# Kernel tuning notes

Hardware: AMD Instinct MI355X
Metric: run time of the kernel (lower is better)

Reference implementation:

```python
import jax, jax.numpy as jnp
import numpy as np

MODES = 256
WIDTH = 64
T_HIST = 1
T_FUT = 1
BATCH = 64
S = 8192


def setup_inputs() -> dict:
    key = jax.random.key(0)
    ks = jax.random.split(key, 12)
    scale = 1.0 / (WIDTH * WIDTH)
    inp = {
        "u": jax.random.normal(ks[0], (BATCH, S, T_HIST), dtype=jnp.float32),
        # lifting layer: Linear(T_HIST+1 -> WIDTH), stored [in, out]
        "fc0_w": jax.random.normal(ks[1], (T_HIST + 1, WIDTH), dtype=jnp.float32) * 0.5,
        "fc0_b": jax.random.normal(ks[2], (WIDTH,), dtype=jnp.float32) * 0.1,
        # 4 spectral conv layers, complex weights stored as real/imag parts
        "sw_r": scale * jax.random.uniform(ks[3], (4, WIDTH, WIDTH, MODES), dtype=jnp.float32),
        "sw_i": scale * jax.random.uniform(ks[4], (4, WIDTH, WIDTH, MODES), dtype=jnp.float32),
        # 4 pointwise (1x1 conv) layers: weight [out,in], bias [out]
        "pw_w": jax.random.normal(ks[5], (4, WIDTH, WIDTH), dtype=jnp.float32) * (1.0 / np.sqrt(WIDTH)),
        "pw_b": jax.random.normal(ks[6], (4, WIDTH), dtype=jnp.float32) * 0.1,
        # projection head
        "fc1_w": jax.random.normal(ks[7], (WIDTH, 128), dtype=jnp.float32) * (1.0 / np.sqrt(WIDTH)),
        "fc1_b": jax.random.normal(ks[8], (128,), dtype=jnp.float32) * 0.1,
        "fc2_w": jax.random.normal(ks[9], (128, T_FUT), dtype=jnp.float32) * (1.0 / np.sqrt(128)),
        "fc2_b": jax.random.normal(ks[10], (T_FUT,), dtype=jnp.float32) * 0.1,
    }
    return inp


def _spectral_conv(x, wr, wi):
    # x: [b, c_in, s] real; weights: [c_in, c_out, MODES] (real/imag parts)
    s = x.shape[-1]
    xf = jnp.fft.rfft(x)                     # [b, c_in, s//2+1] complex
    w = wr + 1j * wi
    om = jnp.einsum('bix,iox->box', xf[:, :, :MODES], w)  # [b, c_out, MODES]
    out_ft = jnp.zeros((x.shape[0], wr.shape[1], s // 2 + 1), dtype=om.dtype)
    out_ft = out_ft.at[:, :, :MODES].set(om)
    return jnp.fft.irfft(out_ft, n=s)        # [b, c_out, s] real


def reference(u, fc0_w, fc0_b, sw_r, sw_i, pw_w, pw_b, fc1_w, fc1_b, fc2_w, fc2_b):
    b, s, _ = u.shape
    grid = jnp.broadcast_to(jnp.linspace(0.0, 1.0, s, dtype=u.dtype)[None, :, None], (b, s, 1))
    x = jnp.concatenate([u, grid], axis=-1)              # [b, s, 2]
    x = x @ fc0_w + fc0_b                                # [b, s, W]
    x = jnp.transpose(x, (0, 2, 1))                      # [b, W, s]
    for l in range(4):
        x1 = _spectral_conv(x, sw_r[l], sw_i[l])
        x2 = jnp.einsum('oi,bis->bos', pw_w[l], x) + pw_b[l][None, :, None]
        x = x1 + x2
        if l < 3:
            x = jax.nn.gelu(x, approximate=False)
    x = jnp.transpose(x, (0, 2, 1))                      # [b, s, W]
    x = jax.nn.gelu(x @ fc1_w + fc1_b, approximate=False)
    x = x @ fc2_w + fc2_b                                # [b, s, T_FUT]
    return x
```

## Files before the change

kernel.cpp:

```cpp
#include <hip/hip_runtime.h>
#include <hip/hip_bf16.h>
#include <math.h>

#define BB 64
#define CC 64
#define SS 8192
#define HS 4096
#define NMODE 256
#define KK2 512

typedef __attribute__((ext_vector_type(8))) short short8;
typedef __attribute__((ext_vector_type(16))) float f32x16;

__device__ __forceinline__ float gelu_exact(float v) {
    return 0.5f * v * (1.0f + erff(v * 0.7071067811865476f));
}
__device__ __forceinline__ float b2f(ushort u) {
    return __uint_as_float(((unsigned int)u) << 16);
}
__device__ __forceinline__ ushort f2b(float v) {
    __hip_bfloat16 h = __float2bfloat16(v);
    return *(ushort*)&h;
}
__device__ __forceinline__ void split2(float v, ushort& h, ushort& l) {
    h = f2b(v);
    l = f2b(v - b2f(h));
}
__device__ __forceinline__ int colk(int c) {
    return (c < 256) ? (c & ~1) : (((c - 256) & ~1) | 1);
}
__device__ __forceinline__ void dma16(const ushort* g, ushort* l) {
    __builtin_amdgcn_global_load_lds((const __attribute__((address_space(1))) void*)g,
                                     (__attribute__((address_space(3))) void*)l, 16, 0, 0);
}

__global__ void build_T1p(ushort* __restrict__ h, ushort* __restrict__ l) {
    int c = blockIdx.x;
    int n = blockIdx.y * 256 + threadIdx.x;
    int k = colk(c), ri = c & 1;
    int m = (n * k) & (SS - 1);
    float th = (float)m * (6.283185307179586476925f / (float)SS);
    float s, co;
    sincosf(th, &s, &co);
    float v = ri ? -s : co;
    ushort hh, ll;
    split2(v, hh, ll);
    h[(size_t)c * HS + n] = hh;
    l[(size_t)c * HS + n] = ll;
}

__global__ void build_T2r(ushort* __restrict__ h, ushort* __restrict__ l) {
    int n = blockIdx.x;
    int c = blockIdx.y * 256 + threadIdx.x;
    int k = colk(c), ri = c & 1;
    int m = (n * k) & (SS - 1);
    float th = (float)m * (6.283185307179586476925f / (float)SS);
    float s, co;
    sincosf(th, &s, &co);
    float v = ri ? -s : co;
    ushort hh, ll;
    split2(v, hh, ll);
    h[(size_t)n * KK2 + c] = hh;
    l[(size_t)n * KK2 + c] = ll;
}

__global__ void zero_xf(float* __restrict__ p) {
    size_t i = ((size_t)blockIdx.x * 256 + threadIdx.x) * 4;
    *(float4*)&p[i] = make_float4(0.f, 0.f, 0.f, 0.f);
}

__global__ void lift_kernel(const float* __restrict__ u, const float* __restrict__ w0,
                            const float* __restrict__ b0, ushort* __restrict__ Eh,
                            ushort* __restrict__ El, ushort* __restrict__ Oh,
                            ushort* __restrict__ Ol) {
    int n = blockIdx.x * 256 + threadIdx.x;
    int c = blockIdx.y;
    int b = blockIdx.z;
    float g1 = (float)n * (1.0f / (float)(SS - 1));
    float g2 = (float)(n + HS) * (1.0f / (float)(SS - 1));
    float v1 = u[b * SS + n] * w0[c] + g1 * w0[CC + c] + b0[c];
    float v2 = u[b * SS + n + HS] * w0[c] + g2 * w0[CC + c] + b0[c];
    float E = v1 + v2, O = v1 - v2;
    ushort hh, ll;
    size_t idx = (size_t)(b * CC + c) * HS + n;
    split2(E, hh, ll);
    Eh[idx] = hh;
    El[idx] = ll;
    split2(O, hh, ll);
    Oh[idx] = hh;
    Ol[idx] = ll;
}

__global__ __launch_bounds__(256, 3) void dft_mfma(
    const ushort* __restrict__ Eh, const ushort* __restrict__ El,
    const ushort* __restrict__ Oh, const ushort* __restrict__ Ol,
    const ushort* __restrict__ t1h, const ushort* __restrict__ t1l,
    float* __restrict__ Xf) {
    __shared__ __align__(16) ushort SM[16384];
    ushort* As_h = SM;
    ushort* As_l = SM + 4096;
    ushort* Bs_h = SM + 8192;
    ushort* Bs_l = SM + 12288;
    const int t = threadIdx.x;
    const int L = blockIdx.x;
    const int gq = L >> 5, j = L & 31;
    const int c0 = (j >> 3) * 128;
    const int m0 = ((gq & 3) * 8 + (j & 7)) * 128;
    const int kz = (gq >> 2) * 1024;
    const ushort* __restrict__ Ahp = (c0 < 256) ? Eh : Oh;
    const ushort* __restrict__ Alp = (c0 < 256) ? El : Ol;
    const int lane = t & 63, w = t >> 6;
    const int wm = (w >> 1) * 64, wn = (w & 1) * 64;
    const int l32 = lane & 31, lh = lane >> 5;
    const int sr = t >> 1, sh = (t & 1) * 16;
    const int g0 = (t & 1) * 2;
    const int d0 = ((g0 + 0) * 128 + sr) * 8;
    const int d1 = ((g0 + 1) * 128 + sr) * 8;

    f32x16 acc[2][2];
#pragma unroll
    for (int i = 0; i < 2; i++)
#pragma unroll
        for (int jj = 0; jj < 2; jj++) acc[i][jj] = (f32x16)0.f;

    const size_t arow = (size_t)(m0 + sr) * HS;
    const size_t brow = (size_t)(c0 + sr) * HS;
    const int kend = kz + 1024;

    short8 a0h, a1h, a0l, a1l, b0h, b1h, b0l, b1l;
    {
        const size_t ga = arow + kz + sh;
        const size_t gb = brow + kz + sh;
        a0h = *(const short8*)&Ahp[ga];
        a1h = *(const short8*)&Ahp[ga + 8];
        a0l = *(const short8*)&Alp[ga];
        a1l = *(const short8*)&Alp[ga + 8];
        b0h = *(const short8*)&t1h[gb];
        b1h = *(const short8*)&t1h[gb + 8];
        b0l = *(const short8*)&t1l[gb];
        b1l = *(const short8*)&t1l[gb + 8];
    }
    for (int kt = kz; kt < kend; kt += 32) {
        __syncthreads();
        *(short8*)&As_h[d0] = a0h;
        *(short8*)&As_h[d1] = a1h;
        *(short8*)&As_l[d0] = a0l;
        *(short8*)&As_l[d1] = a1l;
        *(short8*)&Bs_h[d0] = b0h;
        *(short8*)&Bs_h[d1] = b1h;
        *(short8*)&Bs_l[d0] = b0l;
        *(short8*)&Bs_l[d1] = b1l;
        __syncthreads();
        const int ktn = (kt + 32 < kend) ? kt + 32 : kz;
        const size_t ga = arow + ktn + sh;
        const size_t gb = brow + ktn + sh;
        a0h = *(const short8*)&Ahp[ga];
        a1h = *(const short8*)&Ahp[ga + 8];
        a0l = *(const short8*)&Alp[ga];
        a1l = *(const short8*)&Alp[ga + 8];
        b0h = *(const short8*)&t1h[gb];
        b1h = *(const short8*)&t1h[gb + 8];
        b0l = *(const short8*)&t1l[gb];
        b1l = *(const short8*)&t1l[gb + 8];
#pragma unroll
        for (int s2 = 0; s2 < 2; s2++) {
            const int kg = s2 * 2 + lh;
            short8 ah[2], al[2], bh2[2], bl2[2];
#pragma unroll
            for (int mt = 0; mt < 2; mt++) {
                int off = (kg * 128 + wm + mt * 32 + l32) * 8;
                ah[mt] = *(const short8*)&As_h[off];
                al[mt] = *(const short8*)&As_l[off];
            }
#pragma unroll
            for (int nt = 0; nt < 2; nt++) {
                int off = (kg * 128 + wn + nt * 32 + l32) * 8;
                bh2[nt] = *(const short8*)&Bs_h[off];
                bl2[nt] = *(const short8*)&Bs_l[off];
            }
#pragma unroll
            for (int nt = 0; nt < 2; nt++)
#pragma unroll
                for (int mt = 0; mt < 2; mt++) {
                    acc[mt][nt] = __builtin_amdgcn_mfma_f32_32x32x16_bf16(ah[mt], bh2[nt], acc[mt][nt], 0, 0, 0);
                    acc[mt][nt] = __builtin_amdgcn_mfma_f32_32x32x16_bf16(ah[mt], bl2[nt], acc[mt][nt], 0, 0, 0);
                    acc[mt][nt] = __builtin_amdgcn_mfma_f32_32x32x16_bf16(al[mt], bh2[nt], acc[mt][nt], 0, 0, 0);
                }
        }
    }
#pragma unroll
    for (int mt = 0; mt < 2; mt++)
#pragma unroll
        for (int nt = 0; nt < 2; nt++) {
            int col = c0 + wn + nt * 32 + l32;
#pragma unroll
            for (int reg = 0; reg < 16; reg++) {
                int row = m0 + wm + mt * 32 + (reg & 3) + 8 * (reg >> 2) + 4 * lh;
                atomicAdd(&Xf[(size_t)row * KK2 + col], acc[mt][nt][reg]);
            }
        }
}

__global__ __launch_bounds__(256) void mode_mix(const float* __restrict__ Xf,
                                                const float* __restrict__ swr,
                                                const float* __restrict__ swi,
                                                ushort* __restrict__ omh,
                                                ushort* __restrict__ oml, int l) {
    int k = threadIdx.x;
    int bg = blockIdx.x * 2;
    int og = blockIdx.y * 2;
    const int cp = ((k & 1) << 8) | ((k >> 1) << 1);
    float ar[2][2] = {}, ai[2][2] = {};
#pragma unroll 2
    for (int i = 0; i < CC; i++) {
        float2 x0 = *(const float2*)&Xf[((size_t)(bg + 0) * CC + i) * KK2 + cp];
        float2 x1 = *(const float2*)&Xf[((size_t)(bg + 1) * CC + i) * KK2 + cp];
        size_t wb = ((size_t)(l * CC + i) * CC + og) * NMODE + k;
        float wr0 = swr[wb], wi0 = swi[wb];
        float wr1 = swr[wb + NMODE], wi1 = swi[wb + NMODE];
        ar[0][0] += x0.x * wr0 - x0.y * wi0;
        ai[0][0] += x0.x * wi0 + x0.y * wr0;
        ar[0][1] += x0.x * wr1 - x0.y * wi1;
        ai[0][1] += x0.x * wi1 + x0.y * wr1;
        ar[1][0] += x1.x * wr0 - x1.y * wi0;
        ai[1][0] += x1.x * wi0 + x1.y * wr0;
        ar[1][1] += x1.x * wr1 - x1.y * wi1;
        ai[1][1] += x1.x * wi1 + x1.y * wr1;
    }
    float ck = (k == 0) ? (1.0f / (float)SS) : (2.0f / (float)SS);
#pragma unroll
    for (int b2 = 0; b2 < 2; b2++)
#pragma unroll
        for (int oo = 0; oo < 2; oo++) {
            float re = ar[b2][oo] * ck;
            float im = ai[b2][oo] * ck;
            ushort hr, lr2, hi2, li2;
            split2(re, hr, lr2);
            split2(im, hi2, li2);
            size_t base = ((size_t)(bg + b2) * CC + og + oo) * KK2 + cp;
            *(ushort2*)&omh[base] = make_ushort2(hr, hi2);
            *(ushort2*)&oml[base] = make_ushort2(lr2, li2);
        }
}

__global__ __launch_bounds__(256, 2) void inv_mfma(
    const ushort* __restrict__ omh, const ushort* __restrict__ oml,
    const ushort* __restrict__ t2h, const ushort* __restrict__ t2l,
    const float* __restrict__ pww, const float* __restrict__ pwb,
    ushort* __restrict__ Eh, ushort* __restrict__ El,
    ushort* __restrict__ Oh, ushort* __restrict__ Ol, int l, int gel) {
    __shared__ __align__(16) ushort SM[16384];
    ushort* As_h = SM;
    ushort* As_l = SM + 4096;
    ushort* Bs_h = SM + 8192;
    ushort* Bs_l = SM + 12288;
    const int t = threadIdx.x;
    const int n0 = blockIdx.x * 128;
    const int row0 = blockIdx.y * 128;
    const int lane = t & 63, w = t >> 6;
    const int wm = (w >> 1) * 64, wn = (w & 1) * 64;
    const int l32 = lane & 31, lh = lane >> 5;

    f32x16 aP[2][2], aQ[2][2];
#pragma unroll
    for (int i = 0; i < 2; i++)
#pragma unroll
        for (int jj = 0; jj < 2; jj++) {
            aP[i][jj] = (f32x16)0.f;
            aQ[i][jj] = (f32x16)0.f;
        }

    const size_t aoff = (size_t)(row0 + lane) * KK2 + w * 8;
    const size_t boff = (size_t)(n0 + lane) * KK2 + w * 8;
    const size_t rstep = (size_t)64 * KK2;
    ushort* dAh = As_h + w * 1024;
    ushort* dAl = As_l + w * 1024;
    ushort* dBh = Bs_h + w * 1024;
    ushort* dBl = Bs_l + w * 1024;

#pragma unroll
    for (int half = 0; half < 2; half++) {
        for (int hs8 = 0; hs8 < 8; hs8++) {
            const int kt = half * 256 + hs8 * 32;
            dma16(omh + aoff + kt, dAh);
            dma16(omh + aoff + rstep + kt, dAh + 512);
            dma16(oml + aoff + kt, dAl);
            dma16(oml + aoff + rstep + kt, dAl + 512);
            dma16(t2h + boff + kt, dBh);
            dma16(t2h + boff + rstep + kt, dBh + 512);
            dma16(t2l + boff + kt, dBl);
            dma16(t2l + boff + rstep + kt, dBl + 512);
            __syncthreads();
#pragma unroll
            for (int s2 = 0; s2 < 2; s2++) {
                const int kg = s2 * 2 + lh;
                short8 ah[2], al[2], bh2[2], bl2[2];
#pragma unroll
                for (int mt = 0; mt < 2; mt++) {
                    int off = (kg * 128 + wm + mt * 32 + l32) * 8;
                    ah[mt] = *(const short8*)&As_h[off];
                    al[mt] = *(const short8*)&As_l[off];
                }
#pragma unroll
                for (int nt = 0; nt < 2; nt++) {
                    int off = (kg * 128 + wn + nt * 32 + l32) * 8;
                    bh2[nt] = *(const short8*)&Bs_h[off];
                    bl2[nt] = *(const short8*)&Bs_l[off];
                }
#pragma unroll
                for (int nt = 0; nt < 2; nt++)
#pragma unroll
                    for (int mt = 0; mt < 2; mt++) {
                        f32x16* ac = half ? &aQ[mt][nt] : &aP[mt][nt];
                        *ac = __builtin_amdgcn_mfma_f32_32x32x16_bf16(ah[mt], bh2[nt], *ac, 0, 0, 0);
                        *ac = __builtin_amdgcn_mfma_f32_32x32x16_bf16(ah[mt], bl2[nt], *ac, 0, 0, 0);
                        *ac = __builtin_amdgcn_mfma_f32_32x32x16_bf16(al[mt], bh2[nt], *ac, 0, 0, 0);
                    }
            }
            __syncthreads();
        }
    }
#pragma unroll
    for (int mt = 0; mt < 2; mt++)
#pragma unroll
        for (int nt = 0; nt < 2; nt++) {
            f32x16 p = aP[mt][nt];
            aP[mt][nt] = p + aQ[mt][nt];
            aQ[mt][nt] = p - aQ[mt][nt];
        }
    short8 pah[4][2], pal[4][2];
#pragma unroll
    for (int ks = 0; ks < 4; ks++)
#pragma unroll
        for (int mt = 0; mt < 2; mt++) {
            const float* pp = &pww[(size_t)(l * CC + mt * 32 + l32) * CC + ks * 16 + lh * 8];
            float4 pa = *(const float4*)pp;
            float4 pb = *(const float4*)(pp + 4);
            float pv[8] = {pa.x, pa.y, pa.z, pa.w, pb.x, pb.y, pb.z, pb.w};
#pragma unroll
            for (int e = 0; e < 8; e++) {
                ushort h2, l2;
                split2(0.5f * pv[e], h2, l2);
                pah[ks][mt][e] = (short)h2;
                pal[ks][mt][e] = (short)l2;
            }
        }
    const size_t xsrc = (size_t)(row0 + (w >> 1) * 64 + (w & 1) * 32 + (lane >> 4)) * HS +
                        n0 + (lane & 15) * 8;
    ushort* dX = SM + w * 4096;
    const int bsw = w >> 1;
    const ushort* const srcs[4] = {Eh, El, Oh, Ol};
#pragma unroll
    for (int r = 0; r < 4; r++) {
        const ushort* src = srcs[r];
        const bool isO = (r >= 2), isHi = !(r & 1);
        __syncthreads();
#pragma unroll
        for (int q = 0; q < 8; q++) dma16(src + xsrc + (size_t)q * 4 * HS, dX + q * 512);
        __syncthreads();
#pragma unroll
        for (int ks = 0; ks < 4; ks++) {
            short8 bf[2], nbf[2];
#pragma unroll
            for (int nt = 0; nt < 2; nt++) {
                const int rb = (bsw * 64 + ks * 16 + lh * 8) * 128 + wn + nt * 32 + l32;
#pragma unroll
                for (int jj = 0; jj < 8; jj++) bf[nt][jj] = (short)SM[rb + jj * 128];
                if (isO) {
#pragma unroll
                    for (int jj = 0; jj < 8; jj++)
                        nbf[nt][jj] = (short)(bf[nt][jj] ^ (short)0x8000);
                }
            }
#pragma unroll
            for (int nt = 0; nt < 2; nt++)
#pragma unroll
                for (int mt = 0; mt < 2; mt++) {
                    aP[mt][nt] = __builtin_amdgcn_mfma_f32_32x32x16_bf16(pah[ks][mt], bf[nt], aP[mt][nt], 0, 0, 0);
                    aQ[mt][nt] = __builtin_amdgcn_mfma_f32_32x32x16_bf16(pah[ks][mt], isO ? nbf[nt] : bf[nt], aQ[mt][nt], 0, 0, 0);
                    if (isHi) {
                        aP[mt][nt] = __builtin_amdgcn_mfma_f32_32x32x16_bf16(pal[ks][mt], bf[nt], aP[mt][nt], 0, 0, 0);
                        aQ[mt][nt] = __builtin_amdgcn_mfma_f32_32x32x16_bf16(pal[ks][mt], isO ? nbf[nt] : bf[nt], aQ[mt][nt], 0, 0, 0);
                    }
                }
        }
    }
#pragma unroll
    for (int mt = 0; mt < 2; mt++)
#pragma unroll
        for (int nt = 0; nt < 2; nt++)
#pragma unroll
            for (int reg = 0; reg < 16; reg++) {
                int roffs = (reg & 3) + 8 * (reg >> 2) + 4 * lh;
                float bias = pwb[l * CC + mt * 32 + roffs];
                float uu = aP[mt][nt][reg] + bias;
                float vv = aQ[mt][nt][reg] + bias;
                if (gel) {
                    uu = gelu_exact(uu);
                    vv = gelu_exact(vv);
                }
                float EE = uu + vv, OO = uu - vv;
                ushort h2, l2;
                size_t gg = (size_t)(row0 + wm + mt * 32 + roffs) * HS + n0 + wn + nt * 32 + l32;
                split2(EE, h2, l2);
                Eh[gg] = h2;
                El[gg] = l2;
                split2(OO, h2, l2);
                Oh[gg] = h2;
                Ol[gg] = l2;
            }
}

__global__ __launch_bounds__(256, 3) void head_kernel(
    const ushort* __restrict__ Eh, const ushort* __restrict__ El,
    const ushort* __restrict__ Oh, const ushort* __restrict__ Ol,
    const float* __restrict__ w1, const float* __restrict__ b1,
    const float* __restrict__ w2, const float* __restrict__ b2,
    float* __restrict__ out) {
    __shared__ __align__(16) ushort Xh[4096];
    __shared__ __align__(16) ushort Xl[4096];
    __shared__ __align__(16) ushort Wh[8192];
    __shared__ __align__(16) ushort Wl[8192];
    __shared__ float part[4][64];
    const int b = blockIdx.y;
    const int n0 = blockIdx.x * 64;
    const int t = threadIdx.x;
    const float sg = (n0 < HS) ? 0.5f : -0.5f;
    const int nc = n0 & (HS - 1);
    {
        int c = t >> 2, nq = t & 3;
        size_t gx = (size_t)(b * CC + c) * HS + nc + nq * 16;
        short8 eh0 = *(const short8*)&Eh[gx], eh1 = *(const short8*)&Eh[gx + 8];
        short8 el0 = *(const short8*)&El[gx], el1 = *(const short8*)&El[gx + 8];
        short8 oh0 = *(const short8*)&Oh[gx], oh1 = *(const short8*)&Oh[gx + 8];
        short8 ol0 = *(const short8*)&Ol[gx], ol1 = *(const short8*)&Ol[gx + 8];
        const int base = (c >> 3) * 64, ce = c & 7;
#pragma unroll
        for (int e = 0; e < 8; e++) {
            float e0 = b2f((ushort)eh0[e]) + b2f((ushort)el0[e]);
            float o0 = b2f((ushort)oh0[e]) + b2f((ushort)ol0[e]);
            float e1 = b2f((ushort)eh1[e]) + b2f((ushort)el1[e]);
            float o1 = b2f((ushort)oh1[e]) + b2f((ushort)ol1[e]);
            float x0 = 0.5f * e0 + sg * o0;
            float x1 = 0.5f * e1 + sg * o1;
            ushort hh, ll;
            int na = nq * 16 + e, nb = nq * 16 + 8 + e;
            split2(x0, hh, ll);
            Xh[(base + na) * 8 + ce] = hh;
            Xl[(base + na) * 8 + ce] = ll;
            split2(x1, hh, ll);
            Xh[(base + nb) * 8 + ce] = hh;
            Xl[(base + nb) * 8 + ce] = ll;
        }
    }
#pragma unroll
    for (int q = 0; q < 8; q++) {
        int idx = q * 1024 + t * 4;
        float4 v = *(const float4*)&w1[idx];
        int c = idx >> 7, j0 = idx & 127;
        const int base = (c >> 3) * 128, ce = c & 7;
        float vv[4] = {v.x, v.y, v.z, v.w};
#pragma unroll
        for (int e = 0; e < 4; e++) {
            ushort hh, ll;
            split2(vv[e], hh, ll);
            Wh[(base + j0 + e) * 8 + ce] = hh;
            Wl[(base + j0 + e) * 8 + ce] = ll;
        }
    }
    __syncthreads();
    const int lane = t & 63, w = t >> 6;
    const int l32 = lane & 31, lh = lane >> 5;
    f32x16 acc[2];
    acc[0] = (f32x16)0.f;
    acc[1] = (f32x16)0.f;
#pragma unroll
    for (int ks = 0; ks < 4; ks++) {
        const int kg = ks * 2 + lh;
        short8 axh[2], axl[2];
#pragma unroll
        for (int mt = 0; mt < 2; mt++) {
            int off = (kg * 64 + mt * 32 + l32) * 8;
            axh[mt] = *(const short8*)&Xh[off];
            axl[mt] = *(const short8*)&Xl[off];
        }
        int offb = (kg * 128 + w * 32 + l32) * 8;
        short8 bwh = *(const short8*)&Wh[offb];
        short8 bwl = *(const short8*)&Wl[offb];
#pragma unroll
        for (int mt = 0; mt < 2; mt++) {
            acc[mt] = __builtin_amdgcn_mfma_f32_32x32x16_bf16(axh[mt], bwh, acc[mt], 0, 0, 0);
            acc[mt] = __builtin_amdgcn_mfma_f32_32x32x16_bf16(axh[mt], bwl, acc[mt], 0, 0, 0);
            acc[mt] = __builtin_amdgcn_mfma_f32_32x32x16_bf16(axl[mt], bwh, acc[mt], 0, 0, 0);
        }
    }
    const float bias1 = b1[w * 32 + l32];
    const float w2v = w2[w * 32 + l32];
#pragma unroll
    for (int mt = 0; mt < 2; mt++)
#pragma unroll
        for (int reg = 0; reg < 16; reg++) {
            float pv = gelu_exact(acc[mt][reg] + bias1) * w2v;
            pv += __shfl_xor(pv, 16);
            pv += __shfl_xor(pv, 8);
            pv += __shfl_xor(pv, 4);
            pv += __shfl_xor(pv, 2);
            pv += __shfl_xor(pv, 1);
            if (l32 == 0)
                part[w][mt * 32 + (reg & 3) + 8 * (reg >> 2) + 4 * lh] = pv;
        }
    __syncthreads();
    if (t < 64)
        out[b * SS + n0 + t] = part[0][t] + part[1][t] + part[2][t] + part[3][t] + b2[0];
}

extern "C" void kernel_launch(void* const* d_in, const int* in_sizes, int n_in,
                              void* d_out, int out_size, void* d_ws, size_t ws_size,
                              hipStream_t stream) {
    (void)in_sizes; (void)n_in; (void)out_size; (void)ws_size;
    const float* u = (const float*)d_in[0];
    const float* fc0_w = (const float*)d_in[1];
    const float* fc0_b = (const float*)d_in[2];
    const float* sw_r = (const float*)d_in[3];
    const float* sw_i = (const float*)d_in[4];
    const float* pw_w = (const float*)d_in[5];
    const float* pw_b = (const float*)d_in[6];
    const float* fc1_w = (const float*)d_in[7];
    const float* fc1_b = (const float*)d_in[8];
    const float* fc2_w = (const float*)d_in[9];
    const float* fc2_b = (const float*)d_in[10];
    float* out = (float*)d_out;

    char* ws = (char*)d_ws;
    ushort* Eh = (ushort*)ws;
    ushort* El = (ushort*)(ws + 33554432);
    ushort* Oh = (ushort*)(ws + 67108864);
    ushort* Ol = (ushort*)(ws + 100663296);
    ushort* t1h = (ushort*)(ws + 134217728);
    ushort* t1l = (ushort*)(ws + 138412032);
    ushort* t2h = (ushort*)(ws + 142606336);
    ushort* t2l = (ushort*)(ws + 146800640);
    ushort* omh = (ushort*)(ws + 150994944);
    ushort* oml = (ushort*)(ws + 155189248);
    float* Xf = (float*)(ws + 159383552);

    build_T1p<<<dim3(KK2, HS / 256), 256, 0, stream>>>(t1h, t1l);
    build_T2r<<<dim3(HS, KK2 / 256), 256, 0, stream>>>(t2h, t2l);
    lift_kernel<<<dim3(HS / 256, CC, BB), 256, 0, stream>>>(u, fc0_w, fc0_b, Eh, El,
                                                            Oh, Ol);
    for (int l = 0; l < 4; l++) {
        zero_xf<<<dim3(2048), 256, 0, stream>>>(Xf);
        dft_mfma<<<dim3(512), 256, 0, stream>>>(Eh, El, Oh, Ol, t1h, t1l, Xf);
        mode_mix<<<dim3(BB / 2, CC / 2), 256, 0, stream>>>(Xf, sw_r, sw_i, omh, oml, l);
        inv_mfma<<<dim3(HS / 128, 32), 256, 0, stream>>>(
            omh, oml, t2h, t2l, pw_w, pw_b, Eh, El, Oh, Ol, l, (l < 3) ? 1 : 0);
    }
    head_kernel<<<dim3(SS / 64, BB), 256, 0, stream>>>(Eh, El, Oh, Ol, fc1_w, fc1_b,
                                                       fc2_w, fc2_b, out);
}
```

Before: 1.402 ms.

## Swap MFMA operand roles in head kernel and restructure LDS staging

The head kernel now feeds fc1 weights as the A operand and activations as B, so each lane's accumulator registers run along the hidden dimension. The projection to the output can then be summed mostly within a thread, which replaces the 5-step shuffle reduction per register with a single xor-32 shuffle. The activation and weight staging is rewritten so each thread builds whole short8 vectors and writes them to LDS as vector stores instead of scattered 16-bit stores. In exchange, global loads of the activations become scalar 16-bit reads strided by channel, and b1/w2 are read per register, which may add global load traffic.

```diff
diff --git a/kernel.cpp b/kernel.cpp
--- a/kernel.cpp
+++ b/kernel.cpp
@@ -425,90 +425,81 @@
     const int b = blockIdx.y;
     const int n0 = blockIdx.x * 64;
     const int t = threadIdx.x;
+    const int lane = t & 63, w = t >> 6;
+    const int l32 = lane & 31, lh = lane >> 5;
     const float sg = (n0 < HS) ? 0.5f : -0.5f;
     const int nc = n0 & (HS - 1);
     {
-        int c = t >> 2, nq = t & 3;
-        size_t gx = (size_t)(b * CC + c) * HS + nc + nq * 16;
-        short8 eh0 = *(const short8*)&Eh[gx], eh1 = *(const short8*)&Eh[gx + 8];
-        short8 el0 = *(const short8*)&El[gx], el1 = *(const short8*)&El[gx + 8];
-        short8 oh0 = *(const short8*)&Oh[gx], oh1 = *(const short8*)&Oh[gx + 8];
-        short8 ol0 = *(const short8*)&Ol[gx], ol1 = *(const short8*)&Ol[gx + 8];
-        const int base = (c >> 3) * 64, ce = c & 7;
-#pragma unroll
-        for (int e = 0; e < 8; e++) {
-            float e0 = b2f((ushort)eh0[e]) + b2f((ushort)el0[e]);
-            float o0 = b2f((ushort)oh0[e]) + b2f((ushort)ol0[e]);
-            float e1 = b2f((ushort)eh1[e]) + b2f((ushort)el1[e]);
-            float o1 = b2f((ushort)oh1[e]) + b2f((ushort)ol1[e]);
-            float x0 = 0.5f * e0 + sg * o0;
-            float x1 = 0.5f * e1 + sg * o1;
+        const int n = lane;
+        const size_t gx = (size_t)(b * CC + w * 16) * HS + nc + n;
+        short8 fh[2], fl[2];
+#pragma unroll
+        for (int cc = 0; cc < 16; cc++) {
+            size_t g = gx + (size_t)cc * HS;
+            float e = b2f(Eh[g]) + b2f(El[g]);
+            float o = b2f(Oh[g]) + b2f(Ol[g]);
+            float x = 0.5f * e + sg * o;
             ushort hh, ll;
-            int na = nq * 16 + e, nb = nq * 16 + 8 + e;
-            split2(x0, hh, ll);
-            Xh[(base + na) * 8 + ce] = hh;
-            Xl[(base + na) * 8 + ce] = ll;
-            split2(x1, hh, ll);
-            Xh[(base + nb) * 8 + ce] = hh;
-            Xl[(base + nb) * 8 + ce] = ll;
-        }
-    }
-#pragma unroll
-    for (int q = 0; q < 8; q++) {
-        int idx = q * 1024 + t * 4;
-        float4 v = *(const float4*)&w1[idx];
-        int c = idx >> 7, j0 = idx & 127;
-        const int base = (c >> 3) * 128, ce = c & 7;
-        float vv[4] = {v.x, v.y, v.z, v.w};
-#pragma unroll
-        for (int e = 0; e < 4; e++) {
-            ushort hh, ll;
-            split2(vv[e], hh, ll);
-            Wh[(base + j0 + e) * 8 + ce] = hh;
-            Wl[(base + j0 + e) * 8 + ce] = ll;
+            split2(x, hh, ll);
+            fh[cc >> 3][cc & 7] = (short)hh;
+            fl[cc >> 3][cc & 7] = (short)ll;
+        }
+        const int kg0 = w * 2;
+#pragma unroll
+        for (int q = 0; q < 2; q++) {
+            *(short8*)&Xh[((kg0 + q) * 64 + n) * 8] = fh[q];
+            *(short8*)&Xl[((kg0 + q) * 64 + n) * 8] = fl[q];
+        }
+    }
+    {
+        const int j = t & 127, half = t >> 7;
+#pragma unroll
+        for (int q = 0; q < 4; q++) {
+            const int kg = half * 4 + q;
+            short8 fh, fl;
+#pragma unroll
+            for (int e = 0; e < 8; e++) {
+                int c = kg * 8 + e;
+                ushort hh, ll;
+                split2(w1[c * 128 + j], hh, ll);
+                fh[e] = (short)hh;
+                fl[e] = (short)ll;
+            }
+            *(short8*)&Wh[(kg * 128 + j) * 8] = fh;
+            *(short8*)&Wl[(kg * 128 + j) * 8] = fl;
         }
     }
     __syncthreads();
-    const int lane = t & 63, w = t >> 6;
-    const int l32 = lane & 31, lh = lane >> 5;
     f32x16 acc[2];
     acc[0] = (f32x16)0.f;
     acc[1] = (f32x16)0.f;
 #pragma unroll
     for (int ks = 0; ks < 4; ks++) {
         const int kg = ks * 2 + lh;
-        short8 axh[2], axl[2];
-#pragma unroll
-        for (int mt = 0; mt < 2; mt++) {
-            int off = (kg * 64 + mt * 32 + l32) * 8;
-            axh[mt] = *(const short8*)&Xh[off];
-            axl[mt] = *(const short8*)&Xl[off];
-        }
-        int offb = (kg * 128 + w * 32 + l32) * 8;
-        short8 bwh = *(const short8*)&Wh[offb];
-        short8 bwl = *(const short8*)&Wl[offb];
-#pragma unroll
-        for (int mt = 0; mt < 2; mt++) {
-            acc[mt] = __builtin_amdgcn_mfma_f32_32x32x16_bf16(axh[mt], bwh, acc[mt], 0, 0, 0);
-            acc[mt] = __builtin_amdgcn_mfma_f32_32x32x16_bf16(axh[mt], bwl, acc[mt], 0, 0, 0);
-            acc[mt] = __builtin_amdgcn_mfma_f32_32x32x16_bf16(axl[mt], bwh, acc[mt], 0, 0, 0);
-        }
-    }
-    const float bias1 = b1[w * 32 + l32];
-    const float w2v = w2[w * 32 + l32];
-#pragma unroll
-    for (int mt = 0; mt < 2; mt++)
+        const int offa = (kg * 128 + w * 32 + l32) * 8;
+        short8 awh = *(const short8*)&Wh[offa];
+        short8 awl = *(const short8*)&Wl[offa];
+#pragma unroll
+        for (int nt = 0; nt < 2; nt++) {
+            const int offb = (kg * 64 + nt * 32 + l32) * 8;
+            short8 bxh = *(const short8*)&Xh[offb];
+            short8 bxl = *(const short8*)&Xl[offb];
+            acc[nt] = __builtin_amdgcn_mfma_f32_32x32x16_bf16(awh, bxh, acc[nt], 0, 0, 0);
+            acc[nt] = __builtin_amdgcn_mfma_f32_32x32x16_bf16(awh, bxl, acc[nt], 0, 0, 0);
+            acc[nt] = __builtin_amdgcn_mfma_f32_32x32x16_bf16(awl, bxh, acc[nt], 0, 0, 0);
+        }
+    }
+#pragma unroll
+    for (int nt = 0; nt < 2; nt++) {
+        float s = 0.f;
 #pragma unroll
         for (int reg = 0; reg < 16; reg++) {
-            float pv = gelu_exact(acc[mt][reg] + bias1) * w2v;
-            pv += __shfl_xor(pv, 16);
-            pv += __shfl_xor(pv, 8);
-            pv += __shfl_xor(pv, 4);
-            pv += __shfl_xor(pv, 2);
-            pv += __shfl_xor(pv, 1);
-            if (l32 == 0)
-                part[w][mt * 32 + (reg & 3) + 8 * (reg >> 2) + 4 * lh] = pv;
-        }
+            const int j0 = w * 32 + (reg & 3) + 8 * (reg >> 2) + 4 * lh;
+            s += gelu_exact(acc[nt][reg] + b1[j0]) * w2[j0];
+        }
+        s += __shfl_xor(s, 32);
+        part[w][nt * 32 + l32] = s;
+    }
     __syncthreads();
     if (t < 64)
         out[b * SS + n0 + t] = part[0][t] + part[1][t] + part[2][t] + part[3][t] + b2[0];
```

Measured after the change: 1.269 ms. 9.5% less time.
